# Optimization experiments

Measured on AMD Instinct MI355X. Metric: run time of the kernel, lower is better.

Reference implementation:

```python
import jax, jax.numpy as jnp
import numpy as np

SIGMA = 1.0
RADIUS = 3          # Gaussian kernel radius -> kernel size 7
TAU = 1.0
ITERATIONS = 20
EPS = 1e-6


def _gauss_kernel_1d(sigma: float, radius: int) -> jnp.ndarray:
    x = jnp.arange(-radius, radius + 1, dtype=jnp.float32)
    k = jnp.exp(-0.5 * (x / sigma) ** 2)
    return k / k.sum()


def _smooth(v: jnp.ndarray, k1d: jnp.ndarray) -> jnp.ndarray:
    """Separable Gaussian smoothing of a (1, C, D, H, W) field, 'same' padding."""
    C = v.shape[1]
    r = (k1d.size - 1) // 2
    for ax in range(3):
        shape = [1, 1, 1]
        shape[ax] = k1d.size
        ker = jnp.tile(k1d.reshape((1, 1) + tuple(shape)), (C, 1, 1, 1, 1))
        pad = [(r, r) if i == ax else (0, 0) for i in range(3)]
        v = jax.lax.conv_general_dilated(
            v, ker, window_strides=(1, 1, 1), padding=pad,
            dimension_numbers=('NCDHW', 'OIDHW', 'NCDHW'),
            feature_group_count=C)
    return v


def _warp(image: jnp.ndarray, disp: jnp.ndarray) -> jnp.ndarray:
    """Trilinear warp of (1,1,D,H,W) image by voxel displacement (1,3,D,H,W)."""
    D, H, W = image.shape[2:]
    gd, gh, gw = jnp.meshgrid(
        jnp.arange(D, dtype=disp.dtype),
        jnp.arange(H, dtype=disp.dtype),
        jnp.arange(W, dtype=disp.dtype), indexing='ij')
    coords = [gd + disp[0, 0], gh + disp[0, 1], gw + disp[0, 2]]
    warped = jax.scipy.ndimage.map_coordinates(image[0, 0], coords, order=1, mode='nearest')
    return warped[None, None]


def _spatial_gradient(img: jnp.ndarray) -> jnp.ndarray:
    # img: (D, H, W) -> (3, D, H, W), central differences
    return jnp.stack(jnp.gradient(img))


def _demon_forces_dual(warped, fixed, fixed_grad):
    # warped/fixed: (1,1,D,H,W); dual gradient = mean of moving/fixed gradients
    diff = (warped - fixed)[0, 0]                      # (D,H,W)
    g = 0.5 * (_spatial_gradient(warped[0, 0]) + fixed_grad)  # (3,D,H,W)
    denom = (g ** 2).sum(axis=0) + diff ** 2           # (D,H,W)
    f = jnp.where(denom > EPS, diff * g / denom, 0.0)  # (3,D,H,W)
    return f[None]                                     # (1,3,D,H,W)


def setup_inputs() -> dict:
    key = jax.random.key(0)
    k1, k2 = jax.random.split(key)
    shape = (1, 1, 128, 128, 128)
    moving_image = jax.random.uniform(k1, shape, dtype=jnp.float32)
    fixed_image = jax.random.uniform(k2, shape, dtype=jnp.float32)
    return {"moving_image": moving_image, "fixed_image": fixed_image}


def reference(moving_image, fixed_image):
    kernel = _gauss_kernel_1d(SIGMA, RADIUS)
    fixed_grad = _spatial_gradient(fixed_image[0, 0])
    vf0 = jnp.zeros((1, 3) + moving_image.shape[2:], dtype=moving_image.dtype)

    def step(vf, _):
        warped = _warp(moving_image, vf)
        forces = _demon_forces_dual(warped, fixed_image, fixed_grad)
        vf = _smooth(vf + TAU * forces, kernel)
        return vf, None

    vf, _ = jax.lax.scan(step, vf0, None, length=ITERATIONS)
    return vf
```

## Files before the change

### kernel.cpp

```cpp
#include <hip/hip_runtime.h>

static constexpr int DIM = 128;
static constexpr int N = DIM * DIM * DIM;
static constexpr int ITERS = 20;
static constexpr float EPS = 1e-6f;

#define W0 0.39905028f
#define W1 0.24203624f
#define W2 0.05400559f
#define W3 0.00443305f

__device__ __forceinline__ int clamp_i(int v, int lo, int hi) {
    return min(max(v, lo), hi);
}

#define ROWS 22
#define SSTR 132
#define SC(c, r) ((((c) * ROWS) + (r)) * SSTR)

template <bool FIRST>
__global__ __launch_bounds__(256, 4) void forces_xy_kernel(const float* __restrict__ wpd,
                                                           const float* __restrict__ fix,
                                                           const float* __restrict__ vf,
                                                           float* __restrict__ u2) {
    int b = blockIdx.x;
    int z  = b >> 3;
    int y0 = (b & 7) << 4;

    __shared__ float S[3 * ROWS * SSTR];

    for (int e = threadIdx.x; e < ROWS * 32; e += 256) {
        int x4 = e & 31;
        int r  = e >> 5;
        int gy = y0 + r - 3;
        float4 rz = make_float4(0, 0, 0, 0);
        float4 ry = make_float4(0, 0, 0, 0);
        float4 rx = make_float4(0, 0, 0, 0);
        if (gy >= 0 && gy < 128) {
            int idx = (z << 14) + (gy << 7) + (x4 << 2);
            int xb = x4 << 2;

            float4 wc4 = *(const float4*)(wpd + idx);
            float4 fc4 = *(const float4*)(fix + idx);

            int iyp = (gy < 127) ? idx + 128   : idx;
            int iym = (gy > 0)   ? idx - 128   : idx;
            int izp = (z < 127)  ? idx + 16384 : idx;
            int izm = (z > 0)    ? idx - 16384 : idx;

            float4 wyp = *(const float4*)(wpd + iyp), wym = *(const float4*)(wpd + iym);
            float4 wzp = *(const float4*)(wpd + izp), wzm = *(const float4*)(wpd + izm);
            float4 fyp = *(const float4*)(fix + iyp), fym = *(const float4*)(fix + iym);
            float4 fzp = *(const float4*)(fix + izp), fzm = *(const float4*)(fix + izm);

            float wl = (xb > 0)   ? wpd[idx - 1] : 0.0f;
            float wr = (xb < 124) ? wpd[idx + 4] : 0.0f;
            float fl = (xb > 0)   ? fix[idx - 1] : 0.0f;
            float fr = (xb < 124) ? fix[idx + 4] : 0.0f;

            float wcv[4] = {wc4.x, wc4.y, wc4.z, wc4.w};
            float fcv[4] = {fc4.x, fc4.y, fc4.z, fc4.w};
            float wypv[4] = {wyp.x, wyp.y, wyp.z, wyp.w};
            float wymv[4] = {wym.x, wym.y, wym.z, wym.w};
            float wzpv[4] = {wzp.x, wzp.y, wzp.z, wzp.w};
            float wzmv[4] = {wzm.x, wzm.y, wzm.z, wzm.w};
            float fypv[4] = {fyp.x, fyp.y, fyp.z, fyp.w};
            float fymv[4] = {fym.x, fym.y, fym.z, fym.w};
            float fzpv[4] = {fzp.x, fzp.y, fzp.z, fzp.w};
            float fzmv[4] = {fzm.x, fzm.y, fzm.z, fzm.w};

            float4 vz4 = FIRST ? make_float4(0, 0, 0, 0) : *(const float4*)(vf + idx);
            float4 vy4 = FIRST ? make_float4(0, 0, 0, 0) : *(const float4*)(vf + N + idx);
            float4 vx4 = FIRST ? make_float4(0, 0, 0, 0) : *(const float4*)(vf + 2 * N + idx);
            float vzv[4] = {vz4.x, vz4.y, vz4.z, vz4.w};
            float vyv[4] = {vy4.x, vy4.y, vy4.z, vy4.w};
            float vxv[4] = {vx4.x, vx4.y, vx4.z, vx4.w};

            float ozv[4], oyv[4], oxv[4];
#pragma unroll
            for (int i = 0; i < 4; ++i) {
                float wc = wcv[i], fc = fcv[i];
                float diff = wc - fc;

                float gwz = (z == 0)   ? (wzpv[i] - wc)
                          : (z == 127) ? (wc - wzmv[i])
                          : 0.5f * (wzpv[i] - wzmv[i]);
                float gfz = (z == 0)   ? (fzpv[i] - fc)
                          : (z == 127) ? (fc - fzmv[i])
                          : 0.5f * (fzpv[i] - fzmv[i]);
                float grz = 0.5f * (gwz + gfz);

                float gwy = (gy == 0)   ? (wypv[i] - wc)
                          : (gy == 127) ? (wc - wymv[i])
                          : 0.5f * (wypv[i] - wymv[i]);
                float gfy = (gy == 0)   ? (fypv[i] - fc)
                          : (gy == 127) ? (fc - fymv[i])
                          : 0.5f * (fypv[i] - fymv[i]);
                float gry = 0.5f * (gwy + gfy);

                float wleft  = (i == 0) ? wl : wcv[i - 1];
                float wright = (i == 3) ? wr : wcv[i + 1];
                float fleft  = (i == 0) ? fl : fcv[i - 1];
                float fright = (i == 3) ? fr : fcv[i + 1];
                int xi = xb + i;
                float gwx = (xi == 0)   ? (wright - wc)
                          : (xi == 127) ? (wc - wleft)
                          : 0.5f * (wright - wleft);
                float gfx = (xi == 0)   ? (fright - fc)
                          : (xi == 127) ? (fc - fleft)
                          : 0.5f * (fright - fleft);
                float grx = 0.5f * (gwx + gfx);

                float denom = grz * grz + gry * gry + grx * grx + diff * diff;
                float s = (denom > EPS) ? (diff / denom) : 0.0f;
                ozv[i] = vzv[i] + s * grz;
                oyv[i] = vyv[i] + s * gry;
                oxv[i] = vxv[i] + s * grx;
            }
            rz = make_float4(ozv[0], ozv[1], ozv[2], ozv[3]);
            ry = make_float4(oyv[0], oyv[1], oyv[2], oyv[3]);
            rx = make_float4(oxv[0], oxv[1], oxv[2], oxv[3]);
        }

        float4 vch[3] = {rz, ry, rx};
#pragma unroll
        for (int c = 0; c < 3; ++c) {
            float4 v0 = vch[c];
            float4 m1, p1;
            m1.x = __shfl_up(v0.x, 1);  m1.y = __shfl_up(v0.y, 1);
            m1.z = __shfl_up(v0.z, 1);  m1.w = __shfl_up(v0.w, 1);
            p1.x = __shfl_down(v0.x, 1); p1.y = __shfl_down(v0.y, 1);
            p1.z = __shfl_down(v0.z, 1); p1.w = __shfl_down(v0.w, 1);
            if (x4 == 0)  m1 = make_float4(0, 0, 0, 0);
            if (x4 == 31) p1 = make_float4(0, 0, 0, 0);
            float w[12] = {m1.x, m1.y, m1.z, m1.w,
                           v0.x, v0.y, v0.z, v0.w,
                           p1.x, p1.y, p1.z, p1.w};
            float o[4];
#pragma unroll
            for (int i = 0; i < 4; ++i) {
                o[i] = W3 * (w[i + 1] + w[i + 7]) + W2 * (w[i + 2] + w[i + 6])
                     + W1 * (w[i + 3] + w[i + 5]) + W0 * w[i + 4];
            }
            *(float4*)(S + SC(c, r) + (x4 << 2)) = make_float4(o[0], o[1], o[2], o[3]);
        }
    }
    __syncthreads();

    for (int e = threadIdx.x; e < 16 * 32 * 3; e += 256) {
        int x4 = e & 31;
        int t2 = e >> 5;
        int y  = t2 & 15;
        int c  = t2 >> 4;
        const float* base = S + SC(c, y) + (x4 << 2);
        float4 v0 = *(const float4*)(base);
        float4 v1 = *(const float4*)(base + 1 * SSTR);
        float4 v2 = *(const float4*)(base + 2 * SSTR);
        float4 v3 = *(const float4*)(base + 3 * SSTR);
        float4 v4 = *(const float4*)(base + 4 * SSTR);
        float4 v5 = *(const float4*)(base + 5 * SSTR);
        float4 v6 = *(const float4*)(base + 6 * SSTR);
        float4 acc;
        acc.x = W3 * (v0.x + v6.x) + W2 * (v1.x + v5.x) + W1 * (v2.x + v4.x) + W0 * v3.x;
        acc.y = W3 * (v0.y + v6.y) + W2 * (v1.y + v5.y) + W1 * (v2.y + v4.y) + W0 * v3.y;
        acc.z = W3 * (v0.z + v6.z) + W2 * (v1.z + v5.z) + W1 * (v2.z + v4.z) + W0 * v3.z;
        acc.w = W3 * (v0.w + v6.w) + W2 * (v1.w + v5.w) + W1 * (v2.w + v4.w) + W0 * v3.w;
        *(float4*)(u2 + (size_t)c * N + ((size_t)z << 14) + ((y0 + y) << 7) + (x4 << 2)) = acc;
    }
}

template <bool DO_WARP>
__global__ __launch_bounds__(256, 4) void zblur_warp_kernel(const float* __restrict__ u2,
                                                            const float* __restrict__ mov,
                                                            float* __restrict__ vf,
                                                            float* __restrict__ warped) {
    int k  = blockIdx.x & 7;
    int j  = blockIdx.x >> 3;
    int lb = ((j & 15) << 6) + (k << 3) + (j >> 4);
    int g  = lb * 256 + threadIdx.x;
    int col = g & 16383;
    int zc  = g >> 14;
    int z0  = zc << 3;
    int x = col & 127, y = col >> 7;

    float bz[3][8];
#pragma unroll
    for (int c = 0; c < 3; ++c) {
        const float* inp = u2 + (size_t)c * N + col;
        float win[14];
#pragma unroll
        for (int i = 0; i < 14; ++i) {
            int zz = z0 - 3 + i;
            win[i] = (zz >= 0 && zz < 128) ? inp[(size_t)zz << 14] : 0.0f;
        }
#pragma unroll
        for (int k8 = 0; k8 < 8; ++k8) {
            bz[c][k8] = W3 * (win[k8] + win[k8 + 6]) + W2 * (win[k8 + 1] + win[k8 + 5])
                      + W1 * (win[k8 + 2] + win[k8 + 4]) + W0 * win[k8 + 3];
        }
        float* outp = vf + (size_t)c * N + col;
#pragma unroll
        for (int k8 = 0; k8 < 8; ++k8)
            outp[(size_t)(z0 + k8) << 14] = bz[c][k8];
    }

    if (DO_WARP) {
        for (int k8 = 0; k8 < 8; ++k8) {
            int z = z0 + k8;
            float cz = (float)z + bz[0][k8];
            float cy = (float)y + bz[1][k8];
            float cx = (float)x + bz[2][k8];

            float flz = floorf(cz), fly = floorf(cy), flx = floorf(cx);
            float fz = cz - flz, fy = cy - fly, fx = cx - flx;

            int zi = (int)flz, yi = (int)fly, xi = (int)flx;
            int z0c = clamp_i(zi, 0, DIM - 1), z1c = clamp_i(zi + 1, 0, DIM - 1);
            int y0c = clamp_i(yi, 0, DIM - 1), y1c = clamp_i(yi + 1, 0, DIM - 1);
            int x0c = clamp_i(xi, 0, DIM - 1), x1c = clamp_i(xi + 1, 0, DIM - 1);

            int b00 = (z0c << 14) + (y0c << 7);
            int b01 = (z0c << 14) + (y1c << 7);
            int b10 = (z1c << 14) + (y0c << 7);
            int b11 = (z1c << 14) + (y1c << 7);

            float v000 = mov[b00 + x0c], v001 = mov[b00 + x1c];
            float v010 = mov[b01 + x0c], v011 = mov[b01 + x1c];
            float v100 = mov[b10 + x0c], v101 = mov[b10 + x1c];
            float v110 = mov[b11 + x0c], v111 = mov[b11 + x1c];

            float c00 = v000 + fx * (v001 - v000);
            float c01 = v010 + fx * (v011 - v010);
            float c10 = v100 + fx * (v101 - v100);
            float c11 = v110 + fx * (v111 - v110);
            float c0 = c00 + fy * (c01 - c00);
            float c1 = c10 + fy * (c11 - c10);
            warped[((size_t)z << 14) + col] = c0 + fz * (c1 - c0);
        }
    }
}

extern "C" void kernel_launch(void* const* d_in, const int* in_sizes, int n_in,
                              void* d_out, int out_size, void* d_ws, size_t ws_size,
                              hipStream_t stream) {
    const float* mov = (const float*)d_in[0];
    const float* fix = (const float*)d_in[1];
    float* vf = (float*)d_out;
    float* ws = (float*)d_ws;
    float* warped = ws;
    float* u2     = ws + (size_t)N;

    const int BLK = 256;
    const int gridFX = 128 * 8;
    const int gridZW = (N / 8) / BLK;

    forces_xy_kernel<true><<<gridFX, BLK, 0, stream>>>(mov, fix, nullptr, u2);
    zblur_warp_kernel<true><<<gridZW, BLK, 0, stream>>>(u2, mov, vf, warped);

    for (int it = 1; it < ITERS - 1; ++it) {
        forces_xy_kernel<false><<<gridFX, BLK, 0, stream>>>(warped, fix, vf, u2);
        zblur_warp_kernel<true><<<gridZW, BLK, 0, stream>>>(u2, mov, vf, warped);
    }
    forces_xy_kernel<false><<<gridFX, BLK, 0, stream>>>(warped, fix, vf, u2);
    zblur_warp_kernel<false><<<gridZW, BLK, 0, stream>>>(u2, mov, vf, warped);
}
```

Measured before the change: 770.6 us.

## Fuse all demons iterations into one cooperative persistent kernel with grid syncs

Replaces the 40 separate forces/blur kernel launches with a single cooperative kernel of 1024 blocks. It loops over the iterations and separates the phases with grid-wide syncs. The goal is to remove launch gaps and the kernel-boundary drain between phases. The old multi-launch path is kept as a fallback when cooperative launch or occupancy is not enough. The x-direction neighbour loads in the forces phase are also replaced by wavefront shuffles, which relies on the one-sided boundary handling ignoring values that cross row or wavefront edges.

```diff
diff --git a/kernel.cpp b/kernel.cpp
--- a/kernel.cpp
+++ b/kernel.cpp
@@ -1,4 +1,7 @@
 #include <hip/hip_runtime.h>
+#include <hip/hip_cooperative_groups.h>
+
+namespace cg = cooperative_groups;
 
 static constexpr int DIM = 128;
 static constexpr int N = DIM * DIM * DIM;
@@ -17,17 +20,15 @@
 #define ROWS 22
 #define SSTR 132
 #define SC(c, r) ((((c) * ROWS) + (r)) * SSTR)
-
-template <bool FIRST>
-__global__ __launch_bounds__(256, 4) void forces_xy_kernel(const float* __restrict__ wpd,
-                                                           const float* __restrict__ fix,
-                                                           const float* __restrict__ vf,
-                                                           float* __restrict__ u2) {
-    int b = blockIdx.x;
+#define LDS_FLOATS (3 * ROWS * SSTR)
+
+__device__ __forceinline__ void forces_phase(const float* __restrict__ wpd,
+                                             const float* __restrict__ fix,
+                                             const float* __restrict__ vf,
+                                             float* __restrict__ u2,
+                                             float* S, bool first, int b) {
     int z  = b >> 3;
     int y0 = (b & 7) << 4;
-
-    __shared__ float S[3 * ROWS * SSTR];
 
     for (int e = threadIdx.x; e < ROWS * 32; e += 256) {
         int x4 = e & 31;
@@ -53,10 +54,10 @@
             float4 fyp = *(const float4*)(fix + iyp), fym = *(const float4*)(fix + iym);
             float4 fzp = *(const float4*)(fix + izp), fzm = *(const float4*)(fix + izm);
 
-            float wl = (xb > 0)   ? wpd[idx - 1] : 0.0f;
-            float wr = (xb < 124) ? wpd[idx + 4] : 0.0f;
-            float fl = (xb > 0)   ? fix[idx - 1] : 0.0f;
-            float fr = (xb < 124) ? fix[idx + 4] : 0.0f;
+            float wl = __shfl_up(wc4.w, 1);
+            float wr = __shfl_down(wc4.x, 1);
+            float fl = __shfl_up(fc4.w, 1);
+            float fr = __shfl_down(fc4.x, 1);
 
             float wcv[4] = {wc4.x, wc4.y, wc4.z, wc4.w};
             float fcv[4] = {fc4.x, fc4.y, fc4.z, fc4.w};
@@ -69,9 +70,9 @@
             float fzpv[4] = {fzp.x, fzp.y, fzp.z, fzp.w};
             float fzmv[4] = {fzm.x, fzm.y, fzm.z, fzm.w};
 
-            float4 vz4 = FIRST ? make_float4(0, 0, 0, 0) : *(const float4*)(vf + idx);
-            float4 vy4 = FIRST ? make_float4(0, 0, 0, 0) : *(const float4*)(vf + N + idx);
-            float4 vx4 = FIRST ? make_float4(0, 0, 0, 0) : *(const float4*)(vf + 2 * N + idx);
+            float4 vz4 = first ? make_float4(0, 0, 0, 0) : *(const float4*)(vf + idx);
+            float4 vy4 = first ? make_float4(0, 0, 0, 0) : *(const float4*)(vf + N + idx);
+            float4 vx4 = first ? make_float4(0, 0, 0, 0) : *(const float4*)(vf + 2 * N + idx);
             float vzv[4] = {vz4.x, vz4.y, vz4.z, vz4.w};
             float vyv[4] = {vy4.x, vy4.y, vy4.z, vy4.w};
             float vxv[4] = {vx4.x, vx4.y, vx4.z, vx4.w};
@@ -169,13 +170,13 @@
     }
 }
 
-template <bool DO_WARP>
-__global__ __launch_bounds__(256, 4) void zblur_warp_kernel(const float* __restrict__ u2,
-                                                            const float* __restrict__ mov,
-                                                            float* __restrict__ vf,
-                                                            float* __restrict__ warped) {
-    int k  = blockIdx.x & 7;
-    int j  = blockIdx.x >> 3;
+__device__ __forceinline__ void zblur_phase(const float* __restrict__ u2,
+                                            const float* __restrict__ mov,
+                                            float* __restrict__ vf,
+                                            float* __restrict__ warped,
+                                            bool do_warp, int b) {
+    int k  = b & 7;
+    int j  = b >> 3;
     int lb = ((j & 15) << 6) + (k << 3) + (j >> 4);
     int g  = lb * 256 + threadIdx.x;
     int col = g & 16383;
@@ -204,7 +205,7 @@
             outp[(size_t)(z0 + k8) << 14] = bz[c][k8];
     }
 
-    if (DO_WARP) {
+    if (do_warp) {
         for (int k8 = 0; k8 < 8; ++k8) {
             int z = z0 + k8;
             float cz = (float)z + bz[0][k8];
@@ -238,6 +239,41 @@
             warped[((size_t)z << 14) + col] = c0 + fz * (c1 - c0);
         }
     }
+}
+
+__global__ __launch_bounds__(256, 4) void demons_persistent(const float* mov,
+                                                            const float* fix,
+                                                            float* vf,
+                                                            float* warped,
+                                                            float* u2) {
+    cg::grid_group grid = cg::this_grid();
+    __shared__ float S[LDS_FLOATS];
+    int b = blockIdx.x;
+
+    for (int it = 0; it < ITERS; ++it) {
+        bool first = (it == 0);
+        forces_phase(first ? mov : warped, fix, vf, u2, S, first, b);
+        grid.sync();
+        zblur_phase(u2, mov, vf, warped, it < ITERS - 1, b);
+        if (it < ITERS - 1) grid.sync();
+    }
+}
+
+template <bool FIRST>
+__global__ __launch_bounds__(256, 4) void forces_xy_kernel(const float* __restrict__ wpd,
+                                                           const float* __restrict__ fix,
+                                                           const float* __restrict__ vf,
+                                                           float* __restrict__ u2) {
+    __shared__ float S[LDS_FLOATS];
+    forces_phase(wpd, fix, vf, u2, S, FIRST, blockIdx.x);
+}
+
+template <bool DO_WARP>
+__global__ __launch_bounds__(256, 4) void zblur_warp_kernel(const float* __restrict__ u2,
+                                                            const float* __restrict__ mov,
+                                                            float* __restrict__ vf,
+                                                            float* __restrict__ warped) {
+    zblur_phase(u2, mov, vf, warped, DO_WARP, blockIdx.x);
 }
 
 extern "C" void kernel_launch(void* const* d_in, const int* in_sizes, int n_in,
@@ -251,16 +287,33 @@
     float* u2     = ws + (size_t)N;
 
     const int BLK = 256;
-    const int gridFX = 128 * 8;
-    const int gridZW = (N / 8) / BLK;
-
-    forces_xy_kernel<true><<<gridFX, BLK, 0, stream>>>(mov, fix, nullptr, u2);
-    zblur_warp_kernel<true><<<gridZW, BLK, 0, stream>>>(u2, mov, vf, warped);
-
-    for (int it = 1; it < ITERS - 1; ++it) {
-        forces_xy_kernel<false><<<gridFX, BLK, 0, stream>>>(warped, fix, vf, u2);
-        zblur_warp_kernel<true><<<gridZW, BLK, 0, stream>>>(u2, mov, vf, warped);
-    }
-    forces_xy_kernel<false><<<gridFX, BLK, 0, stream>>>(warped, fix, vf, u2);
-    zblur_warp_kernel<false><<<gridZW, BLK, 0, stream>>>(u2, mov, vf, warped);
-}
+    const int GRID = 1024;
+
+    static int coop_ok = -1;
+    if (coop_ok < 0) {
+        int dev = 0;
+        (void)hipGetDevice(&dev);
+        int coop = 0;
+        (void)hipDeviceGetAttribute(&coop, hipDeviceAttributeCooperativeLaunch, dev);
+        int ncu = 0;
+        (void)hipDeviceGetAttribute(&ncu, hipDeviceAttributeMultiprocessorCount, dev);
+        int occ = 0;
+        (void)hipOccupancyMaxActiveBlocksPerMultiprocessor(&occ, demons_persistent, BLK, 0);
+        coop_ok = (coop && (long long)occ * ncu >= GRID) ? 1 : 0;
+    }
+
+    if (coop_ok) {
+        void* args[] = {(void*)&mov, (void*)&fix, (void*)&vf, (void*)&warped, (void*)&u2};
+        (void)hipLaunchCooperativeKernel(demons_persistent, dim3(GRID), dim3(BLK),
+                                         args, 0, stream);
+    } else {
+        forces_xy_kernel<true><<<GRID, BLK, 0, stream>>>(mov, fix, nullptr, u2);
+        zblur_warp_kernel<true><<<GRID, BLK, 0, stream>>>(u2, mov, vf, warped);
+        for (int it = 1; it < ITERS - 1; ++it) {
+            forces_xy_kernel<false><<<GRID, BLK, 0, stream>>>(warped, fix, vf, u2);
+            zblur_warp_kernel<true><<<GRID, BLK, 0, stream>>>(u2, mov, vf, warped);
+        }
+        forces_xy_kernel<false><<<GRID, BLK, 0, stream>>>(warped, fix, vf, u2);
+        zblur_warp_kernel<false><<<GRID, BLK, 0, stream>>>(u2, mov, vf, warped);
+    }
+}
```

Measured after the change: 766.6 us. No clear change (-0.5%).
